# Kernel optimization log

Hardware: AMD Instinct MI355X
Metric: run time of the kernel (lower is better)

## Reference

```python
import jax, jax.numpy as jnp
import numpy as np

EPS_BN = 1e-5
EPS_LN = 1e-5
B_, CIN, COUT, H_, W_ = 8, 64, 128, 64, 64
DSTATE, DCONV, EXPAND = 16, 4, 2
DINNER = EXPAND * COUT            # 256
DTRANK = (COUT + 15) // 16        # 8


def setup_inputs() -> dict:
    key = jax.random.key(0)
    ks = jax.random.split(key, 24)
    g = lambda i, shape, s=0.02: jax.random.normal(ks[i], shape, jnp.float32) * s
    inp = {}
    inp["x"] = jax.random.normal(ks[0], (B_, CIN, H_, W_), jnp.float32)
    # conv-bn-relu x2
    inp["conv1_w"] = g(1, (COUT, CIN, 3, 3), 0.05)
    inp["conv1_b"] = jnp.zeros((COUT,), jnp.float32)
    inp["bn1_g"] = jnp.ones((COUT,), jnp.float32)
    inp["bn1_b"] = jnp.zeros((COUT,), jnp.float32)
    inp["bn1_m"] = g(2, (COUT,), 0.1)
    inp["bn1_v"] = jnp.ones((COUT,), jnp.float32)
    inp["conv2_w"] = g(3, (COUT, COUT, 3, 3), 0.05)
    inp["conv2_b"] = jnp.zeros((COUT,), jnp.float32)
    inp["bn2_g"] = jnp.ones((COUT,), jnp.float32)
    inp["bn2_b"] = jnp.zeros((COUT,), jnp.float32)
    inp["bn2_m"] = g(4, (COUT,), 0.1)
    inp["bn2_v"] = jnp.ones((COUT,), jnp.float32)
    # Mamba params (mamba_ssm defaults: projections bias-free except dt_proj)
    inp["in_proj_w"] = g(5, (2 * DINNER, COUT))
    inp["conv1d_w"] = g(6, (DINNER, 1, DCONV), 0.1)   # depthwise
    inp["conv1d_b"] = jnp.zeros((DINNER,), jnp.float32)
    inp["x_proj_w"] = g(7, (DTRANK + 2 * DSTATE, DINNER))
    inp["dt_proj_w"] = g(8, (DINNER, DTRANK), 0.1)
    inp["dt_proj_b"] = g(9, (DINNER,), 0.5)
    # S4D-real init: A = -[1..d_state] per channel
    A = jnp.tile(jnp.arange(1, DSTATE + 1, dtype=jnp.float32)[None, :], (DINNER, 1))
    inp["A_log"] = jnp.log(A)
    inp["D"] = jnp.ones((DINNER,), jnp.float32)
    inp["out_proj_w"] = g(10, (COUT, DINNER))
    inp["ln_g"] = jnp.ones((COUT,), jnp.float32)
    inp["ln_b"] = jnp.zeros((COUT,), jnp.float32)
    return inp


def _conv3x3(x, w, b):
    y = jax.lax.conv_general_dilated(x, w, (1, 1), ((1, 1), (1, 1)),
                                     dimension_numbers=("NCHW", "OIHW", "NCHW"))
    return y + b[None, :, None, None]


def _bn_eval(x, g, b, m, v):
    inv = jax.lax.rsqrt(v + EPS_BN)
    return (x - m[None, :, None, None]) * (g * inv)[None, :, None, None] + b[None, :, None, None]


def _mamba(x_flat, in_proj_w, conv1d_w, conv1d_b, x_proj_w, dt_proj_w, dt_proj_b, A_log, D, out_proj_w):
    # x_flat: (B, L, C)
    Bsz, L, _ = x_flat.shape
    xz = jnp.einsum("blc,ec->ble", x_flat, in_proj_w)          # (B, L, 2*di)
    xm, z = jnp.split(xz, 2, axis=-1)                           # each (B, L, di)
    # causal depthwise conv1d over time
    xt = jnp.transpose(xm, (0, 2, 1))                           # (B, di, L)
    xt = jax.lax.conv_general_dilated(xt, conv1d_w, (1,), ((DCONV - 1, 0),),
                                      dimension_numbers=("NCH", "OIH", "NCH"),
                                      feature_group_count=DINNER)
    xt = xt + conv1d_b[None, :, None]
    x_ssm = jax.nn.silu(jnp.transpose(xt, (0, 2, 1)))           # (B, L, di)
    xdb = jnp.einsum("bld,ed->ble", x_ssm, x_proj_w)            # (B, L, dt_rank+2*ds)
    dt_r = xdb[..., :DTRANK]
    Bm = xdb[..., DTRANK:DTRANK + DSTATE]                       # (B, L, ds)
    Cm = xdb[..., DTRANK + DSTATE:]                             # (B, L, ds)
    dt = jax.nn.softplus(jnp.einsum("blr,dr->bld", dt_r, dt_proj_w) + dt_proj_b)
    A = -jnp.exp(A_log)                                         # (di, ds)

    def step(h, inp):
        dt_t, B_t, C_t, x_t = inp                               # (B,di) (B,ds) (B,ds) (B,di)
        dA = jnp.exp(dt_t[:, :, None] * A)                      # (B, di, ds)
        h = dA * h + (dt_t * x_t)[:, :, None] * B_t[:, None, :]
        y = jnp.einsum("bds,bs->bd", h, C_t)
        return h, y

    xs = (jnp.swapaxes(dt, 0, 1), jnp.swapaxes(Bm, 0, 1),
          jnp.swapaxes(Cm, 0, 1), jnp.swapaxes(x_ssm, 0, 1))
    h0 = jnp.zeros((Bsz, DINNER, DSTATE), jnp.float32)
    _, ys = jax.lax.scan(step, h0, xs)                          # (L, B, di)
    y = jnp.swapaxes(ys, 0, 1) + D * x_ssm
    y = y * jax.nn.silu(z)
    return jnp.einsum("bld,od->blo", y, out_proj_w)             # (B, L, C)


def reference(x, conv1_w, conv1_b, bn1_g, bn1_b, bn1_m, bn1_v,
              conv2_w, conv2_b, bn2_g, bn2_b, bn2_m, bn2_v,
              in_proj_w, conv1d_w, conv1d_b, x_proj_w, dt_proj_w, dt_proj_b,
              A_log, D, out_proj_w, ln_g, ln_b):
    h = jax.nn.relu(_bn_eval(_conv3x3(x, conv1_w, conv1_b), bn1_g, bn1_b, bn1_m, bn1_v))
    h = jax.nn.relu(_bn_eval(_conv3x3(h, conv2_w, conv2_b), bn2_g, bn2_b, bn2_m, bn2_v))
    Bsz, C, Hh, Ww = h.shape
    seq = jnp.transpose(h, (0, 2, 3, 1)).reshape(Bsz, Hh * Ww, C)
    seq = _mamba(seq, in_proj_w, conv1d_w, conv1d_b, x_proj_w,
                 dt_proj_w, dt_proj_b, A_log, D, out_proj_w)
    # LayerNorm over channels
    mu = jnp.mean(seq, axis=-1, keepdims=True)
    var = jnp.mean(jnp.square(seq - mu), axis=-1, keepdims=True)
    seq = (seq - mu) * jax.lax.rsqrt(var + EPS_LN) * ln_g + ln_b
    return jnp.transpose(seq.reshape(Bsz, Hh, Ww, C), (0, 3, 1, 2))
```

## Files before the change

### kernel.cpp

```cpp
#include <hip/hip_runtime.h>
#include <hip/hip_bf16.h>


typedef __attribute__((ext_vector_type(8))) short bf16x8;
typedef __attribute__((ext_vector_type(4))) float f32x4;

#define DEV __device__ __forceinline__

constexpr float LOG2E = 1.44269504088896f;

DEV float siluf(float v) {
  return v * __builtin_amdgcn_rcpf(1.f + __expf(-v));
}

DEV unsigned short f2bf(float f) {
  __hip_bfloat16 h = __float2bfloat16(f);
  return *reinterpret_cast<unsigned short*>(&h);
}

DEV float bf2f(unsigned short u) {
  unsigned int x = (unsigned int)u << 16;
  return __builtin_bit_cast(float, x);
}

DEV void gll16(const void* g, void* l) {
  __builtin_amdgcn_global_load_lds(
      (const __attribute__((address_space(1))) void*)g,
      (__attribute__((address_space(3))) void*)l, 16, 0, 0);
}

constexpr int NC = 128;
constexpr int CL = 32;

__global__ __launch_bounds__(256) void nchw2nhwc_bf16(
    const float* __restrict__ X, unsigned short* __restrict__ Xb)
{
  __shared__ float t[64][65];
  const int by = blockIdx.x;
  const int b = by >> 6, y = by & 63;
  const int tid = threadIdx.x;
  for (int i = tid; i < 4096; i += 256) {
    int c = i >> 6, xx = i & 63;
    t[c][xx] = X[(((size_t)b * 64 + c) * 64 + y) * 64 + xx];
  }
  __syncthreads();
  for (int i = tid; i < 4096; i += 256) {
    int xx = i >> 6, c = i & 63;
    Xb[(((size_t)(b * 66 + y + 1) * 66) + xx + 1) * 64 + c] = f2bf(t[c][xx]);
  }
}

template<int CI>
__global__ void convw_prep(const float* __restrict__ W,
                           unsigned short* __restrict__ Wb)
{
  int idx = blockIdx.x * 256 + threadIdx.x;
  if (idx >= 128 * 9 * CI) return;
  int co = idx / (9 * CI), r = idx % (9 * CI);
  int t = r / CI, ci = r % CI;
  Wb[idx] = f2bf(W[((size_t)co * CI + ci) * 9 + t]);
}

__global__ void f32_to_bf16(const float* __restrict__ A,
                            unsigned short* __restrict__ B, int n)
{
  int i = blockIdx.x * 256 + threadIdx.x;
  if (i < n) B[i] = f2bf(A[i]);
}

__global__ void xprojw_prep(const float* __restrict__ W,
                            unsigned short* __restrict__ Wb)
{
  int idx = blockIdx.x * 256 + threadIdx.x;
  if (idx >= 128 * 256) return;
  int r = idx >> 8, c = idx & 255;
  Wb[idx] = (r < 40) ? f2bf(W[r * 256 + c]) : (unsigned short)0;
}

template<int CI, int PADOUT>
__global__ __launch_bounds__(256) void conv_mfma(
    const unsigned short* __restrict__ Xp,
    const unsigned short* __restrict__ Wb,
    const float* __restrict__ bc,
    const float* __restrict__ bg, const float* __restrict__ bb,
    const float* __restrict__ bm, const float* __restrict__ bv,
    unsigned short* __restrict__ Y)
{
  constexpr int KC  = 3 * CI / 64;
  constexpr int NCH = 3 * KC;
  __shared__ bf16x8 ldsA[2][512];

  const int lane = threadIdx.x & 63;
  const int wid  = threadIdx.x >> 6;
  const int n0 = wid * 32;
  const int y = blockIdx.x, b = blockIdx.y;
  const int lr = lane & 15, kq = lane >> 4, lk = kq * 8;

  auto stage = [&](int buf, int c) {
    const int dy = c / KC, kc = c - dy * KC;
    const unsigned short* g = Xp
        + (size_t)((b * 66 + y + dy) * 66) * CI
        + (size_t)lane * CI + kc * 64 + wid * 16;
    gll16(g,     &ldsA[buf][(wid * 2) * 64]);
    gll16(g + 8, &ldsA[buf][(wid * 2 + 1) * 64]);
  };

  f32x4 acc[4][2];
  #pragma unroll
  for (int i = 0; i < 4; ++i)
    #pragma unroll
    for (int j = 0; j < 2; ++j) acc[i][j] = f32x4{0.f, 0.f, 0.f, 0.f};

  stage(0, 0);
  __syncthreads();

  #pragma unroll
  for (int c = 0; c < NCH; ++c) {
    if (c + 1 < NCH) stage((c + 1) & 1, c + 1);
    const int dy = c / KC, kc = c - dy * KC;
    bf16x8 bw[2][2];
    #pragma unroll
    for (int t = 0; t < 2; ++t)
      #pragma unroll
      for (int nf = 0; nf < 2; ++nf)
        bw[t][nf] = *reinterpret_cast<const bf16x8*>(
            Wb + (size_t)(n0 + nf * 16 + lr) * (9 * CI)
               + dy * 3 * CI + kc * 64 + t * 32 + lk);
    const bf16x8* Ab = ldsA[c & 1];
    #pragma unroll
    for (int t = 0; t < 2; ++t)
      #pragma unroll
      for (int mf = 0; mf < 4; ++mf) {
        bf16x8 afr = Ab[(t * 4 + kq) * 64 + mf * 16 + lr];
        #pragma unroll
        for (int nf = 0; nf < 2; ++nf)
          acc[mf][nf] = __builtin_amdgcn_mfma_f32_16x16x32_bf16(
              afr, bw[t][nf], acc[mf][nf], 0, 0, 0);
      }
    __syncthreads();
  }

  #pragma unroll
  for (int nf = 0; nf < 2; ++nf) {
    int n = n0 + nf * 16 + lr;
    float aS = bg[n] * rsqrtf(bv[n] + 1e-5f);
    float aB = (bc[n] - bm[n]) * aS + bb[n];
    #pragma unroll
    for (int mf = 0; mf < 4; ++mf)
      #pragma unroll
      for (int i = 0; i < 4; ++i) {
        int m = mf * 16 + kq * 4 + i;
        float v = fmaxf(acc[mf][nf][i] * aS + aB, 0.f);
        if (PADOUT)
          Y[((size_t)(b * 66 + y + 1) * 66 + m + 1) * 128 + n] = f2bf(v);
        else
          Y[((size_t)(b * 4096 + y * 64 + m)) * 128 + n] = f2bf(v);
      }
  }
}

template<int KDIM, int EPI>
__global__ __launch_bounds__(256) void gemm_mfma(
    const unsigned short* __restrict__ A,
    const unsigned short* __restrict__ Wn,
    float* __restrict__ C0, unsigned short* __restrict__ C1b)
{
  constexpr int NCH = KDIM / 64;
  __shared__ bf16x8 ldsA[2][512];

  const int lane = threadIdx.x & 63;
  const int wid  = threadIdx.x >> 6;
  const int m0 = blockIdx.x * 64;
  const int n0 = blockIdx.y * 128 + wid * 32;
  const int lr = lane & 15, kq = lane >> 4, lk = kq * 8;

  bf16x8 bw[NCH][2][2];
  #pragma unroll
  for (int c = 0; c < NCH; ++c)
    #pragma unroll
    for (int t = 0; t < 2; ++t)
      #pragma unroll
      for (int nf = 0; nf < 2; ++nf)
        bw[c][t][nf] = *reinterpret_cast<const bf16x8*>(
            Wn + (size_t)(n0 + nf * 16 + lr) * KDIM + c * 64 + t * 32 + lk);

  auto stage = [&](int buf, int c) {
    const unsigned short* g = A + (size_t)(m0 + lane) * KDIM + c * 64 + wid * 16;
    gll16(g,     &ldsA[buf][(wid * 2) * 64]);
    gll16(g + 8, &ldsA[buf][(wid * 2 + 1) * 64]);
  };

  f32x4 acc[4][2];
  #pragma unroll
  for (int i = 0; i < 4; ++i)
    #pragma unroll
    for (int j = 0; j < 2; ++j) acc[i][j] = f32x4{0.f, 0.f, 0.f, 0.f};

  stage(0, 0);
  __syncthreads();

  #pragma unroll
  for (int c = 0; c < NCH; ++c) {
    if (c + 1 < NCH) stage((c + 1) & 1, c + 1);
    const bf16x8* Ab = ldsA[c & 1];
    #pragma unroll
    for (int t = 0; t < 2; ++t)
      #pragma unroll
      for (int mf = 0; mf < 4; ++mf) {
        bf16x8 afr = Ab[(t * 4 + kq) * 64 + mf * 16 + lr];
        #pragma unroll
        for (int nf = 0; nf < 2; ++nf)
          acc[mf][nf] = __builtin_amdgcn_mfma_f32_16x16x32_bf16(
              afr, bw[c][t][nf], acc[mf][nf], 0, 0, 0);
      }
    __syncthreads();
  }

  #pragma unroll
  for (int nf = 0; nf < 2; ++nf) {
    int n = n0 + nf * 16 + lr;
    #pragma unroll
    for (int mf = 0; mf < 4; ++mf)
      #pragma unroll
      for (int i = 0; i < 4; ++i) {
        int m = m0 + mf * 16 + kq * 4 + i;
        float v = acc[mf][nf][i];
        if (EPI == 0) {
          if (n < 256) C0[(size_t)m * 256 + n] = v;
          else         C1b[(size_t)m * 256 + (n - 256)] = f2bf(v);
        } else if (EPI == 1) {
          C0[(size_t)m * 128 + n] = v;
        } else {
          if (n < 40) C0[(size_t)m * 40 + n] = v;
        }
      }
  }
}

__global__ __launch_bounds__(256) void conv1d_silu(
    const float* __restrict__ xm,
    const float* __restrict__ w,
    const float* __restrict__ bias,
    unsigned short* __restrict__ out)
{
  __shared__ float ws4[4][256];
  __shared__ float bsh[256];
  for (int i = threadIdx.x; i < 1024; i += 256)
    ws4[i >> 8][i & 255] = w[(i & 255) * 4 + (i >> 8)];
  bsh[threadIdx.x] = bias[threadIdx.x];
  __syncthreads();
  const int total = 8 * 4096 * 64;
  for (int idx = blockIdx.x * 256 + threadIdx.x; idx < total;
       idx += gridDim.x * 256) {
    int d4 = idx & 63, t = idx >> 6, l = t & 4095;
    int d = d4 * 4;
    float4 acc = *reinterpret_cast<const float4*>(&bsh[d]);
    #pragma unroll
    for (int j = 0; j < 4; ++j) {
      if (l - 3 + j >= 0) {
        float4 xv = *reinterpret_cast<const float4*>(&xm[(size_t)(t - 3 + j) * 256 + d]);
        float4 wv = *reinterpret_cast<const float4*>(&ws4[j][d]);
        acc.x = fmaf(xv.x, wv.x, acc.x);
        acc.y = fmaf(xv.y, wv.y, acc.y);
        acc.z = fmaf(xv.z, wv.z, acc.z);
        acc.w = fmaf(xv.w, wv.w, acc.w);
      }
    }
    ushort4 o;
    o.x = f2bf(siluf(acc.x)); o.y = f2bf(siluf(acc.y));
    o.z = f2bf(siluf(acc.z)); o.w = f2bf(siluf(acc.w));
    *reinterpret_cast<ushort4*>(&out[(size_t)t * 256 + d]) = o;
  }
}

__global__ __launch_bounds__(256) void scan_pass1(
    const unsigned short* __restrict__ xssm, const float* __restrict__ xdb,
    const float* __restrict__ dtw, const float* __restrict__ dtb,
    const float* __restrict__ A_log,
    float* __restrict__ Q, float* __restrict__ S)
{
  __shared__ __align__(16) float sh[CL][40];
  const int c = blockIdx.x, b = blockIdx.y;
  const int d = threadIdx.x;
  {
    const float4* src = reinterpret_cast<const float4*>(
        &xdb[((size_t)b * 4096 + c * CL) * 40]);
    float4* dst = reinterpret_cast<float4*>(&sh[0][0]);
    for (int i = threadIdx.x; i < CL * 10; i += 256) dst[i] = src[i];
  }
  float4 w0 = *reinterpret_cast<const float4*>(&dtw[d * 8]);
  float4 w1 = *reinterpret_cast<const float4*>(&dtw[d * 8 + 4]);
  const float bdt = dtb[d];
  float An2[16], h[16];
  #pragma unroll
  for (int s = 0; s < 16; ++s) {
    An2[s] = -__expf(A_log[d * 16 + s]) * LOG2E;
    h[s] = 0.f;
  }
  __syncthreads();

  float sdt = 0.f;
  const size_t xbase = ((size_t)b * 4096 + (size_t)c * CL) * 256 + d;
  unsigned short xu = xssm[xbase];
  for (int l = 0; l < CL; ++l) {
    unsigned short xun = (l + 1 < CL) ? xssm[xbase + (size_t)(l + 1) * 256]
                                      : (unsigned short)0;
    const float4* row = reinterpret_cast<const float4*>(sh[l]);
    float4 r0 = row[0], r1 = row[1];
    float acc = bdt;
    acc = fmaf(r0.x, w0.x, acc); acc = fmaf(r0.y, w0.y, acc);
    acc = fmaf(r0.z, w0.z, acc); acc = fmaf(r0.w, w0.w, acc);
    acc = fmaf(r1.x, w1.x, acc); acc = fmaf(r1.y, w1.y, acc);
    acc = fmaf(r1.z, w1.z, acc); acc = fmaf(r1.w, w1.w, acc);
    float dt = (acc > 20.f) ? acc : __logf(1.f + __expf(acc));
    sdt += dt;
    float dtx = dt * bf2f(xu);
    #pragma unroll
    for (int q = 0; q < 4; ++q) {
      float4 Bq = row[2 + q];
      float bb4[4] = {Bq.x, Bq.y, Bq.z, Bq.w};
      #pragma unroll
      for (int j = 0; j < 4; ++j) {
        int s = q * 4 + j;
        float dA = __builtin_amdgcn_exp2f(dt * An2[s]);
        h[s] = fmaf(dA, h[s], dtx * bb4[j]);
      }
    }
    xu = xun;
  }
  float4* q4 = reinterpret_cast<float4*>(
      &Q[(((size_t)b * NC + c) * 256 + d) * 16]);
  #pragma unroll
  for (int q = 0; q < 4; ++q)
    q4[q] = make_float4(h[q * 4], h[q * 4 + 1], h[q * 4 + 2], h[q * 4 + 3]);
  S[((size_t)b * NC + c) * 256 + d] = sdt;
}

__global__ __launch_bounds__(256) void scan_combine(
    float* __restrict__ Q, const float* __restrict__ S,
    const float* __restrict__ A_log)
{
  int g = blockIdx.x * 256 + threadIdx.x;
  int b = g >> 12, d = (g >> 4) & 255, s = g & 15;
  float Aneg = -__expf(A_log[d * 16 + s]);
  float h = 0.f;
  for (int c = 0; c < NC; ++c) {
    size_t qi = (((size_t)b * NC + c) * 256 + d) * 16 + s;
    float q  = Q[qi];
    float sd = S[((size_t)b * NC + c) * 256 + d];
    Q[qi] = h;
    h = fmaf(__expf(Aneg * sd), h, q);
  }
}

__global__ __launch_bounds__(256) void scan_pass2(
    const unsigned short* __restrict__ xssm, const float* __restrict__ xdb,
    const unsigned short* __restrict__ zb,
    const float* __restrict__ dtw, const float* __restrict__ dtb,
    const float* __restrict__ A_log, const float* __restrict__ Dp,
    const float* __restrict__ Hstart, unsigned short* __restrict__ ybf)
{
  __shared__ __align__(16) float sh[CL][40];
  const int c = blockIdx.x, b = blockIdx.y;
  const int d = threadIdx.x;
  {
    const float4* src = reinterpret_cast<const float4*>(
        &xdb[((size_t)b * 4096 + c * CL) * 40]);
    float4* dst = reinterpret_cast<float4*>(&sh[0][0]);
    for (int i = threadIdx.x; i < CL * 10; i += 256) dst[i] = src[i];
  }
  float4 w0 = *reinterpret_cast<const float4*>(&dtw[d * 8]);
  float4 w1 = *reinterpret_cast<const float4*>(&dtw[d * 8 + 4]);
  const float bdt = dtb[d];
  const float Dd = Dp[d];
  float An2[16], h[16];
  const float4* hs4 = reinterpret_cast<const float4*>(
      &Hstart[(((size_t)b * NC + c) * 256 + d) * 16]);
  #pragma unroll
  for (int q = 0; q < 4; ++q) {
    float4 hv = hs4[q];
    h[q * 4 + 0] = hv.x; h[q * 4 + 1] = hv.y;
    h[q * 4 + 2] = hv.z; h[q * 4 + 3] = hv.w;
  }
  #pragma unroll
  for (int s = 0; s < 16; ++s) An2[s] = -__expf(A_log[d * 16 + s]) * LOG2E;
  __syncthreads();

  const size_t xbase = ((size_t)b * 4096 + (size_t)c * CL) * 256 + d;
  unsigned short xu = xssm[xbase], zu = zb[xbase];
  for (int l = 0; l < CL; ++l) {
    unsigned short xun = 0, zun = 0;
    if (l + 1 < CL) {
      xun = xssm[xbase + (size_t)(l + 1) * 256];
      zun = zb[xbase + (size_t)(l + 1) * 256];
    }
    const float4* row = reinterpret_cast<const float4*>(sh[l]);
    float4 r0 = row[0], r1 = row[1];
    float acc = bdt;
    acc = fmaf(r0.x, w0.x, acc); acc = fmaf(r0.y, w0.y, acc);
    acc = fmaf(r0.z, w0.z, acc); acc = fmaf(r0.w, w0.w, acc);
    acc = fmaf(r1.x, w1.x, acc); acc = fmaf(r1.y, w1.y, acc);
    acc = fmaf(r1.z, w1.z, acc); acc = fmaf(r1.w, w1.w, acc);
    float dt = (acc > 20.f) ? acc : __logf(1.f + __expf(acc));
    float xv = bf2f(xu);
    float dtx = dt * xv;
    float yq[4] = {0.f, 0.f, 0.f, 0.f};
    #pragma unroll
    for (int q = 0; q < 4; ++q) {
      float4 Bq = row[2 + q], Cq = row[6 + q];
      float bb4[4] = {Bq.x, Bq.y, Bq.z, Bq.w};
      float cc4[4] = {Cq.x, Cq.y, Cq.z, Cq.w};
      #pragma unroll
      for (int j = 0; j < 4; ++j) {
        int s = q * 4 + j;
        float dA = __builtin_amdgcn_exp2f(dt * An2[s]);
        h[s] = fmaf(dA, h[s], dtx * bb4[j]);
        yq[q] = fmaf(h[s], cc4[j], yq[q]);
      }
    }
    float y = (yq[0] + yq[1]) + (yq[2] + yq[3]);
    y = (y + Dd * xv) * siluf(bf2f(zu));
    ybf[xbase + (size_t)l * 256] = f2bf(y);
    xu = xun; zu = zun;
  }
}

__global__ __launch_bounds__(256) void ln_transpose(
    const float* __restrict__ X,
    const float* __restrict__ g, const float* __restrict__ b,
    float* __restrict__ out)
{
  __shared__ float buf[64][129];
  const int t0 = blockIdx.x * 64;
  const int bb = t0 >> 12, l0 = t0 & 4095;
  const int tid = threadIdx.x;
  for (int idx = tid; idx < 64 * 128; idx += 256)
    buf[idx >> 7][idx & 127] = X[(size_t)t0 * 128 + idx];
  __syncthreads();
  const int tt = tid >> 2, q = tid & 3;
  float s = 0.f, sq = 0.f;
  #pragma unroll
  for (int i = 0; i < 32; ++i) {
    float v = buf[tt][q * 32 + i];
    s += v; sq += v * v;
  }
  s  += __shfl_xor(s, 1);  s  += __shfl_xor(s, 2);
  sq += __shfl_xor(sq, 1); sq += __shfl_xor(sq, 2);
  float mu = s * (1.f / 128.f);
  float var = sq * (1.f / 128.f) - mu * mu;
  float rstd = rsqrtf(fmaxf(var, 0.f) + 1e-5f);
  #pragma unroll
  for (int i = 0; i < 32; ++i) {
    int c = q * 32 + i;
    buf[tt][c] = (buf[tt][c] - mu) * rstd * g[c] + b[c];
  }
  __syncthreads();
  for (int idx = tid; idx < 64 * 128; idx += 256) {
    int c = idx >> 6, t2 = idx & 63;
    out[((size_t)bb * 128 + c) * 4096 + l0 + t2] = buf[t2][c];
  }
}

extern "C" void kernel_launch(void* const* d_in, const int* in_sizes, int n_in,
                              void* d_out, int out_size, void* d_ws, size_t ws_size,
                              hipStream_t stream) {
  const float* x        = (const float*)d_in[0];
  const float* conv1_w  = (const float*)d_in[1];
  const float* conv1_b  = (const float*)d_in[2];
  const float* bn1_g    = (const float*)d_in[3];
  const float* bn1_b    = (const float*)d_in[4];
  const float* bn1_m    = (const float*)d_in[5];
  const float* bn1_v    = (const float*)d_in[6];
  const float* conv2_w  = (const float*)d_in[7];
  const float* conv2_b  = (const float*)d_in[8];
  const float* bn2_g    = (const float*)d_in[9];
  const float* bn2_b    = (const float*)d_in[10];
  const float* bn2_m    = (const float*)d_in[11];
  const float* bn2_v    = (const float*)d_in[12];
  const float* in_proj_w  = (const float*)d_in[13];
  const float* conv1d_w   = (const float*)d_in[14];
  const float* conv1d_b   = (const float*)d_in[15];
  const float* x_proj_w   = (const float*)d_in[16];
  const float* dt_proj_w  = (const float*)d_in[17];
  const float* dt_proj_b  = (const float*)d_in[18];
  const float* A_log      = (const float*)d_in[19];
  const float* Dp         = (const float*)d_in[20];
  const float* out_proj_w = (const float*)d_in[21];
  const float* ln_g       = (const float*)d_in[22];
  const float* ln_b       = (const float*)d_in[23];
  float* out = (float*)d_out;

  float* ws_f = (float*)d_ws;
  unsigned short* xbp  = (unsigned short*)ws_f;
  float*          xm   = ws_f;
  unsigned short* ybf  = (unsigned short*)ws_f;
  float*          xdb  = ws_f + 4194304;
  float*          Sbuf = ws_f + 5505024;
  float*          outs = ws_f + 4194304;
  unsigned short* zbu  = (unsigned short*)(ws_f + 8388608);
  unsigned short* xsu  = (unsigned short*)(ws_f + 16777216);
  unsigned short* h1p  = (unsigned short*)(ws_f + 25165824);
  unsigned short* seqb = (unsigned short*)(ws_f + 27396096);
  float*          Qbuf = ws_f + 25165824;
  unsigned short* wb1  = (unsigned short*)(ws_f + 29493248);
  unsigned short* wb2  = (unsigned short*)(ws_f + 29530112);
  unsigned short* win  = (unsigned short*)(ws_f + 29603840);
  unsigned short* wout = (unsigned short*)(ws_f + 29636608);
  unsigned short* xpwb = (unsigned short*)(ws_f + 29652992);

  hipMemsetAsync(xbp, 0, (size_t)8 * 66 * 66 * 64 * 2, stream);
  hipMemsetAsync(h1p, 0, (size_t)8 * 66 * 66 * 128 * 2, stream);

  nchw2nhwc_bf16<<<512, 256, 0, stream>>>(x, xbp);
  convw_prep<64><<<(73728 + 255) / 256, 256, 0, stream>>>(conv1_w, wb1);
  convw_prep<128><<<(147456 + 255) / 256, 256, 0, stream>>>(conv2_w, wb2);
  f32_to_bf16<<<256, 256, 0, stream>>>(in_proj_w, win, 65536);
  f32_to_bf16<<<128, 256, 0, stream>>>(out_proj_w, wout, 32768);
  xprojw_prep<<<128, 256, 0, stream>>>(x_proj_w, xpwb);

  conv_mfma<64, 1><<<dim3(64, 8), 256, 0, stream>>>(
      xbp, wb1, conv1_b, bn1_g, bn1_b, bn1_m, bn1_v, h1p);
  conv_mfma<128, 0><<<dim3(64, 8), 256, 0, stream>>>(
      h1p, wb2, conv2_b, bn2_g, bn2_b, bn2_m, bn2_v, seqb);

  gemm_mfma<128, 0><<<dim3(512, 4), 256, 0, stream>>>(seqb, win, xm, zbu);

  conv1d_silu<<<2048, 256, 0, stream>>>(xm, conv1d_w, conv1d_b, xsu);

  gemm_mfma<256, 2><<<dim3(512, 1), 256, 0, stream>>>(xsu, xpwb, xdb, nullptr);

  scan_pass1<<<dim3(NC, 8), 256, 0, stream>>>(
      xsu, xdb, dt_proj_w, dt_proj_b, A_log, Qbuf, Sbuf);
  scan_combine<<<128, 256, 0, stream>>>(Qbuf, Sbuf, A_log);
  scan_pass2<<<dim3(NC, 8), 256, 0, stream>>>(
      xsu, xdb, zbu, dt_proj_w, dt_proj_b, A_log, Dp, Qbuf, ybf);

  gemm_mfma<256, 1><<<dim3(512, 1), 256, 0, stream>>>(ybf, wout, outs, nullptr);
  ln_transpose<<<512, 256, 0, stream>>>(outs, ln_g, ln_b, out);
}
```

Baseline: 218.9 us.

## Store Mamba intermediates in bf16, merge weight prep, and shorten scan chunks

```diff
diff --git a/kernel.cpp b/kernel.cpp
--- a/kernel.cpp
+++ b/kernel.cpp
@@ -29,8 +29,8 @@
       (__attribute__((address_space(3))) void*)l, 16, 0, 0);
 }
 
-constexpr int NC = 128;
-constexpr int CL = 32;
+constexpr int NC = 256;
+constexpr int CL = 16;
 
 __global__ __launch_bounds__(256) void nchw2nhwc_bf16(
     const float* __restrict__ X, unsigned short* __restrict__ Xb)
@@ -50,31 +50,33 @@
   }
 }
 
-template<int CI>
-__global__ void convw_prep(const float* __restrict__ W,
-                           unsigned short* __restrict__ Wb)
+__global__ __launch_bounds__(256) void prep_all(
+    const float* __restrict__ conv1_w, const float* __restrict__ conv2_w,
+    const float* __restrict__ in_proj_w, const float* __restrict__ out_proj_w,
+    const float* __restrict__ x_proj_w, const float* __restrict__ A_log,
+    unsigned short* __restrict__ wb1, unsigned short* __restrict__ wb2,
+    unsigned short* __restrict__ win, unsigned short* __restrict__ wout,
+    unsigned short* __restrict__ xpwb, float* __restrict__ An2f)
 {
   int idx = blockIdx.x * 256 + threadIdx.x;
-  if (idx >= 128 * 9 * CI) return;
-  int co = idx / (9 * CI), r = idx % (9 * CI);
-  int t = r / CI, ci = r % CI;
-  Wb[idx] = f2bf(W[((size_t)co * CI + ci) * 9 + t]);
-}
-
-__global__ void f32_to_bf16(const float* __restrict__ A,
-                            unsigned short* __restrict__ B, int n)
-{
-  int i = blockIdx.x * 256 + threadIdx.x;
-  if (i < n) B[i] = f2bf(A[i]);
-}
-
-__global__ void xprojw_prep(const float* __restrict__ W,
-                            unsigned short* __restrict__ Wb)
-{
-  int idx = blockIdx.x * 256 + threadIdx.x;
-  if (idx >= 128 * 256) return;
-  int r = idx >> 8, c = idx & 255;
-  Wb[idx] = (r < 40) ? f2bf(W[r * 256 + c]) : (unsigned short)0;
+  if (idx < 73728) {
+    int co = idx / 576, r = idx % 576, t = r >> 6, ci = r & 63;
+    wb1[idx] = f2bf(conv1_w[((size_t)co * 64 + ci) * 9 + t]);
+  } else if (idx < 221184) {
+    int i = idx - 73728;
+    int co = i / 1152, r = i % 1152, t = r >> 7, ci = r & 127;
+    wb2[i] = f2bf(conv2_w[((size_t)co * 128 + ci) * 9 + t]);
+  } else if (idx < 286720) {
+    int i = idx - 221184; win[i] = f2bf(in_proj_w[i]);
+  } else if (idx < 319488) {
+    int i = idx - 286720; wout[i] = f2bf(out_proj_w[i]);
+  } else if (idx < 352256) {
+    int i = idx - 319488; int r = i >> 8, c = i & 255;
+    xpwb[i] = (r < 40) ? f2bf(x_proj_w[r * 256 + c]) : (unsigned short)0;
+  } else if (idx < 356352) {
+    int i = idx - 352256;
+    An2f[i] = -__expf(A_log[i]) * LOG2E;
+  }
 }
 
 template<int CI, int PADOUT>
@@ -163,7 +165,8 @@
 __global__ __launch_bounds__(256) void gemm_mfma(
     const unsigned short* __restrict__ A,
     const unsigned short* __restrict__ Wn,
-    float* __restrict__ C0, unsigned short* __restrict__ C1b)
+    float* __restrict__ C0,
+    unsigned short* __restrict__ Cb0, unsigned short* __restrict__ Cb1)
 {
   constexpr int NCH = KDIM / 64;
   __shared__ bf16x8 ldsA[2][512];
@@ -226,8 +229,8 @@
         int m = m0 + mf * 16 + kq * 4 + i;
         float v = acc[mf][nf][i];
         if (EPI == 0) {
-          if (n < 256) C0[(size_t)m * 256 + n] = v;
-          else         C1b[(size_t)m * 256 + (n - 256)] = f2bf(v);
+          if (n < 256) Cb0[(size_t)m * 256 + n] = f2bf(v);
+          else         Cb1[(size_t)m * 256 + (n - 256)] = f2bf(v);
         } else if (EPI == 1) {
           C0[(size_t)m * 128 + n] = v;
         } else {
@@ -238,7 +241,7 @@
 }
 
 __global__ __launch_bounds__(256) void conv1d_silu(
-    const float* __restrict__ xm,
+    const unsigned short* __restrict__ xm,
     const float* __restrict__ w,
     const float* __restrict__ bias,
     unsigned short* __restrict__ out)
@@ -249,54 +252,66 @@
     ws4[i >> 8][i & 255] = w[(i & 255) * 4 + (i >> 8)];
   bsh[threadIdx.x] = bias[threadIdx.x];
   __syncthreads();
-  const int total = 8 * 4096 * 64;
+  const int total = 32768 * 32;
   for (int idx = blockIdx.x * 256 + threadIdx.x; idx < total;
        idx += gridDim.x * 256) {
-    int d4 = idx & 63, t = idx >> 6, l = t & 4095;
-    int d = d4 * 4;
-    float4 acc = *reinterpret_cast<const float4*>(&bsh[d]);
+    int d8 = idx & 31, t = idx >> 5, l = t & 4095;
+    int d = d8 * 8;
+    float acc[8];
+    #pragma unroll
+    for (int k = 0; k < 8; ++k) acc[k] = bsh[d + k];
     #pragma unroll
     for (int j = 0; j < 4; ++j) {
       if (l - 3 + j >= 0) {
-        float4 xv = *reinterpret_cast<const float4*>(&xm[(size_t)(t - 3 + j) * 256 + d]);
-        float4 wv = *reinterpret_cast<const float4*>(&ws4[j][d]);
-        acc.x = fmaf(xv.x, wv.x, acc.x);
-        acc.y = fmaf(xv.y, wv.y, acc.y);
-        acc.z = fmaf(xv.z, wv.z, acc.z);
-        acc.w = fmaf(xv.w, wv.w, acc.w);
-      }
-    }
-    ushort4 o;
-    o.x = f2bf(siluf(acc.x)); o.y = f2bf(siluf(acc.y));
-    o.z = f2bf(siluf(acc.z)); o.w = f2bf(siluf(acc.w));
-    *reinterpret_cast<ushort4*>(&out[(size_t)t * 256 + d]) = o;
+        uint4 xv = *reinterpret_cast<const uint4*>(
+            &xm[(size_t)(t - 3 + j) * 256 + d]);
+        const unsigned short* xs = reinterpret_cast<const unsigned short*>(&xv);
+        #pragma unroll
+        for (int k = 0; k < 8; ++k)
+          acc[k] = fmaf(bf2f(xs[k]), ws4[j][d + k], acc[k]);
+      }
+    }
+    unsigned int pk[4];
+    #pragma unroll
+    for (int k = 0; k < 4; ++k) {
+      unsigned short lo = f2bf(siluf(acc[2 * k]));
+      unsigned short hi = f2bf(siluf(acc[2 * k + 1]));
+      pk[k] = (unsigned int)lo | ((unsigned int)hi << 16);
+    }
+    *reinterpret_cast<uint4*>(&out[(size_t)t * 256 + d]) =
+        *reinterpret_cast<uint4*>(pk);
   }
 }
 
 __global__ __launch_bounds__(256) void scan_pass1(
     const unsigned short* __restrict__ xssm, const float* __restrict__ xdb,
     const float* __restrict__ dtw, const float* __restrict__ dtb,
-    const float* __restrict__ A_log,
-    float* __restrict__ Q, float* __restrict__ S)
+    const float* __restrict__ An2f,
+    unsigned short* __restrict__ Qb, float* __restrict__ S)
 {
   __shared__ __align__(16) float sh[CL][40];
   const int c = blockIdx.x, b = blockIdx.y;
   const int d = threadIdx.x;
-  {
+  if (threadIdx.x < CL * 10) {
     const float4* src = reinterpret_cast<const float4*>(
         &xdb[((size_t)b * 4096 + c * CL) * 40]);
-    float4* dst = reinterpret_cast<float4*>(&sh[0][0]);
-    for (int i = threadIdx.x; i < CL * 10; i += 256) dst[i] = src[i];
+    reinterpret_cast<float4*>(&sh[0][0])[threadIdx.x] = src[threadIdx.x];
   }
   float4 w0 = *reinterpret_cast<const float4*>(&dtw[d * 8]);
   float4 w1 = *reinterpret_cast<const float4*>(&dtw[d * 8 + 4]);
   const float bdt = dtb[d];
   float An2[16], h[16];
-  #pragma unroll
-  for (int s = 0; s < 16; ++s) {
-    An2[s] = -__expf(A_log[d * 16 + s]) * LOG2E;
-    h[s] = 0.f;
-  }
+  {
+    const f32x4* a2 = reinterpret_cast<const f32x4*>(&An2f[d * 16]);
+    #pragma unroll
+    for (int q = 0; q < 4; ++q) {
+      f32x4 v = a2[q];
+      An2[q * 4 + 0] = v[0]; An2[q * 4 + 1] = v[1];
+      An2[q * 4 + 2] = v[2]; An2[q * 4 + 3] = v[3];
+    }
+  }
+  #pragma unroll
+  for (int s = 0; s < 16; ++s) h[s] = 0.f;
   __syncthreads();
 
   float sdt = 0.f;
@@ -328,28 +343,37 @@
     }
     xu = xun;
   }
-  float4* q4 = reinterpret_cast<float4*>(
-      &Q[(((size_t)b * NC + c) * 256 + d) * 16]);
-  #pragma unroll
-  for (int q = 0; q < 4; ++q)
-    q4[q] = make_float4(h[q * 4], h[q * 4 + 1], h[q * 4 + 2], h[q * 4 + 3]);
+  unsigned int pk[8];
+  #pragma unroll
+  for (int k = 0; k < 8; ++k)
+    pk[k] = (unsigned int)f2bf(h[2 * k]) | ((unsigned int)f2bf(h[2 * k + 1]) << 16);
+  uint4* qp = reinterpret_cast<uint4*>(
+      &Qb[(((size_t)b * NC + c) * 256 + d) * 16]);
+  qp[0] = *reinterpret_cast<uint4*>(pk);
+  qp[1] = *reinterpret_cast<uint4*>(pk + 4);
   S[((size_t)b * NC + c) * 256 + d] = sdt;
 }
 
 __global__ __launch_bounds__(256) void scan_combine(
-    float* __restrict__ Q, const float* __restrict__ S,
-    const float* __restrict__ A_log)
+    unsigned short* __restrict__ Qb, const float* __restrict__ S,
+    const float* __restrict__ An2f)
 {
   int g = blockIdx.x * 256 + threadIdx.x;
   int b = g >> 12, d = (g >> 4) & 255, s = g & 15;
-  float Aneg = -__expf(A_log[d * 16 + s]);
+  float An2 = An2f[d * 16 + s];
+  const size_t qbase = (size_t)b * NC * 4096 + d * 16 + s;
+  const size_t sbase = (size_t)b * NC * 256 + d;
   float h = 0.f;
+  unsigned short qn = Qb[qbase];
+  float sn = S[sbase];
   for (int c = 0; c < NC; ++c) {
-    size_t qi = (((size_t)b * NC + c) * 256 + d) * 16 + s;
-    float q  = Q[qi];
-    float sd = S[((size_t)b * NC + c) * 256 + d];
-    Q[qi] = h;
-    h = fmaf(__expf(Aneg * sd), h, q);
+    float q = bf2f(qn), sd = sn;
+    if (c + 1 < NC) {
+      qn = Qb[qbase + (size_t)(c + 1) * 4096];
+      sn = S[sbase + (size_t)(c + 1) * 256];
+    }
+    Qb[qbase + (size_t)c * 4096] = f2bf(h);
+    h = fmaf(__builtin_amdgcn_exp2f(An2 * sd), h, q);
   }
 }
 
@@ -357,33 +381,42 @@
     const unsigned short* __restrict__ xssm, const float* __restrict__ xdb,
     const unsigned short* __restrict__ zb,
     const float* __restrict__ dtw, const float* __restrict__ dtb,
-    const float* __restrict__ A_log, const float* __restrict__ Dp,
-    const float* __restrict__ Hstart, unsigned short* __restrict__ ybf)
+    const float* __restrict__ An2f, const float* __restrict__ Dp,
+    const unsigned short* __restrict__ Hstart, unsigned short* __restrict__ ybf)
 {
   __shared__ __align__(16) float sh[CL][40];
   const int c = blockIdx.x, b = blockIdx.y;
   const int d = threadIdx.x;
-  {
+  if (threadIdx.x < CL * 10) {
     const float4* src = reinterpret_cast<const float4*>(
         &xdb[((size_t)b * 4096 + c * CL) * 40]);
-    float4* dst = reinterpret_cast<float4*>(&sh[0][0]);
-    for (int i = threadIdx.x; i < CL * 10; i += 256) dst[i] = src[i];
+    reinterpret_cast<float4*>(&sh[0][0])[threadIdx.x] = src[threadIdx.x];
   }
   float4 w0 = *reinterpret_cast<const float4*>(&dtw[d * 8]);
   float4 w1 = *reinterpret_cast<const float4*>(&dtw[d * 8 + 4]);
   const float bdt = dtb[d];
   const float Dd = Dp[d];
   float An2[16], h[16];
-  const float4* hs4 = reinterpret_cast<const float4*>(
-      &Hstart[(((size_t)b * NC + c) * 256 + d) * 16]);
-  #pragma unroll
-  for (int q = 0; q < 4; ++q) {
-    float4 hv = hs4[q];
-    h[q * 4 + 0] = hv.x; h[q * 4 + 1] = hv.y;
-    h[q * 4 + 2] = hv.z; h[q * 4 + 3] = hv.w;
-  }
-  #pragma unroll
-  for (int s = 0; s < 16; ++s) An2[s] = -__expf(A_log[d * 16 + s]) * LOG2E;
+  {
+    const f32x4* a2 = reinterpret_cast<const f32x4*>(&An2f[d * 16]);
+    #pragma unroll
+    for (int q = 0; q < 4; ++q) {
+      f32x4 v = a2[q];
+      An2[q * 4 + 0] = v[0]; An2[q * 4 + 1] = v[1];
+      An2[q * 4 + 2] = v[2]; An2[q * 4 + 3] = v[3];
+    }
+  }
+  {
+    const uint4* hp = reinterpret_cast<const uint4*>(
+        &Hstart[(((size_t)b * NC + c) * 256 + d) * 16]);
+    uint4 h0 = hp[0], h1 = hp[1];
+    const unsigned short* hs = reinterpret_cast<const unsigned short*>(&h0);
+    #pragma unroll
+    for (int s = 0; s < 8; ++s) h[s] = bf2f(hs[s]);
+    const unsigned short* hs2 = reinterpret_cast<const unsigned short*>(&h1);
+    #pragma unroll
+    for (int s = 0; s < 8; ++s) h[8 + s] = bf2f(hs2[s]);
+  }
   __syncthreads();
 
   const size_t xbase = ((size_t)b * 4096 + (size_t)c * CL) * 256 + d;
@@ -492,49 +525,51 @@
 
   float* ws_f = (float*)d_ws;
   unsigned short* xbp  = (unsigned short*)ws_f;
-  float*          xm   = ws_f;
+  unsigned short* xmb  = (unsigned short*)ws_f;
   unsigned short* ybf  = (unsigned short*)ws_f;
   float*          xdb  = ws_f + 4194304;
   float*          Sbuf = ws_f + 5505024;
   float*          outs = ws_f + 4194304;
   unsigned short* zbu  = (unsigned short*)(ws_f + 8388608);
-  unsigned short* xsu  = (unsigned short*)(ws_f + 16777216);
-  unsigned short* h1p  = (unsigned short*)(ws_f + 25165824);
-  unsigned short* seqb = (unsigned short*)(ws_f + 27396096);
-  float*          Qbuf = ws_f + 25165824;
-  unsigned short* wb1  = (unsigned short*)(ws_f + 29493248);
-  unsigned short* wb2  = (unsigned short*)(ws_f + 29530112);
-  unsigned short* win  = (unsigned short*)(ws_f + 29603840);
-  unsigned short* wout = (unsigned short*)(ws_f + 29636608);
-  unsigned short* xpwb = (unsigned short*)(ws_f + 29652992);
+  unsigned short* xsu  = (unsigned short*)(ws_f + 12582912);
+  unsigned short* h1p  = (unsigned short*)(ws_f + 16777216);
+  unsigned short* seqb = (unsigned short*)(ws_f + 19007488);
+  unsigned short* Qb   = (unsigned short*)(ws_f + 16777216);
+  unsigned short* wb1  = (unsigned short*)(ws_f + 25165824);
+  unsigned short* wb2  = (unsigned short*)(ws_f + 25202688);
+  unsigned short* win  = (unsigned short*)(ws_f + 25276416);
+  unsigned short* wout = (unsigned short*)(ws_f + 25309184);
+  unsigned short* xpwb = (unsigned short*)(ws_f + 25325568);
+  float*          An2f = ws_f + 25341952;
 
   hipMemsetAsync(xbp, 0, (size_t)8 * 66 * 66 * 64 * 2, stream);
   hipMemsetAsync(h1p, 0, (size_t)8 * 66 * 66 * 128 * 2, stream);
 
   nchw2nhwc_bf16<<<512, 256, 0, stream>>>(x, xbp);
-  convw_prep<64><<<(73728 + 255) / 256, 256, 0, stream>>>(conv1_w, wb1);
-  convw_prep<128><<<(147456 + 255) / 256, 256, 0, stream>>>(conv2_w, wb2);
-  f32_to_bf16<<<256, 256, 0, stream>>>(in_proj_w, win, 65536);
-  f32_to_bf16<<<128, 256, 0, stream>>>(out_proj_w, wout, 32768);
-  xprojw_prep<<<128, 256, 0, stream>>>(x_proj_w, xpwb);
+  prep_all<<<1392, 256, 0, stream>>>(conv1_w, conv2_w, in_proj_w, out_proj_w,
+                                     x_proj_w, A_log,
+                                     wb1, wb2, win, wout, xpwb, An2f);
 
   conv_mfma<64, 1><<<dim3(64, 8), 256, 0, stream>>>(
       xbp, wb1, conv1_b, bn1_g, bn1_b, bn1_m, bn1_v, h1p);
   conv_mfma<128, 0><<<dim3(64, 8), 256, 0, stream>>>(
       h1p, wb2, conv2_b, bn2_g, bn2_b, bn2_m, bn2_v, seqb);
 
-  gemm_mfma<128, 0><<<dim3(512, 4), 256, 0, stream>>>(seqb, win, xm, zbu);
-
-  conv1d_silu<<<2048, 256, 0, stream>>>(xm, conv1d_w, conv1d_b, xsu);
-
-  gemm_mfma<256, 2><<<dim3(512, 1), 256, 0, stream>>>(xsu, xpwb, xdb, nullptr);
+  gemm_mfma<128, 0><<<dim3(512, 4), 256, 0, stream>>>(
+      seqb, win, nullptr, xmb, zbu);
+
+  conv1d_silu<<<2048, 256, 0, stream>>>(xmb, conv1d_w, conv1d_b, xsu);
+
+  gemm_mfma<256, 2><<<dim3(512, 1), 256, 0, stream>>>(
+      xsu, xpwb, xdb, nullptr, nullptr);
 
   scan_pass1<<<dim3(NC, 8), 256, 0, stream>>>(
-      xsu, xdb, dt_proj_w, dt_proj_b, A_log, Qbuf, Sbuf);
-  scan_combine<<<128, 256, 0, stream>>>(Qbuf, Sbuf, A_log);
+      xsu, xdb, dt_proj_w, dt_proj_b, An2f, Qb, Sbuf);
+  scan_combine<<<128, 256, 0, stream>>>(Qb, Sbuf, An2f);
   scan_pass2<<<dim3(NC, 8), 256, 0, stream>>>(
-      xsu, xdb, zbu, dt_proj_w, dt_proj_b, A_log, Dp, Qbuf, ybf);
-
-  gemm_mfma<256, 1><<<dim3(512, 1), 256, 0, stream>>>(ybf, wout, outs, nullptr);
+      xsu, xdb, zbu, dt_proj_w, dt_proj_b, An2f, Dp, Qb, ybf);
+
+  gemm_mfma<256, 1><<<dim3(512, 1), 256, 0, stream>>>(
+      ybf, wout, outs, nullptr, nullptr);
   ln_transpose<<<512, 256, 0, stream>>>(outs, ln_g, ln_b, out);
 }
```

After: 218.5 us. About the same (-0.2%).
